# Kernel tuning notes

Hardware: AMD Instinct MI355X
Metric: run time of the kernel (lower is better)

The kernel has to match this reference:

```python
import jax, jax.numpy as jnp
import numpy as np

N_NODES = 100000
N_EDGES = 3200000
F_IN = 512
F_HID = 16
F_OUT = 40


def setup_inputs() -> dict:
    key = jax.random.key(0)
    k_x, k_e, k_w1, k_w2 = jax.random.split(key, 4)
    x = jax.random.normal(k_x, (N_NODES, F_IN), dtype=jnp.float32)
    edge_index = jax.random.randint(k_e, (2, N_EDGES), 0, N_NODES, dtype=jnp.int32)
    # Glorot-ish init for GCN weights
    W1 = jax.random.normal(k_w1, (F_IN, F_HID), dtype=jnp.float32) * (1.0 / np.sqrt(F_IN))
    b1 = jnp.zeros((F_HID,), dtype=jnp.float32)
    W2 = jax.random.normal(k_w2, (F_HID, F_OUT), dtype=jnp.float32) * (1.0 / np.sqrt(F_HID))
    b2 = jnp.zeros((F_OUT,), dtype=jnp.float32)
    return {"x": x, "edge_index": edge_index, "W1": W1, "b1": b1, "W2": W2, "b2": b2}


def reference(x, edge_index, W1, b1, W2, b2):
    # Eval-mode forward: dropout is identity.
    n = x.shape[0]
    loops = jnp.arange(n, dtype=edge_index.dtype)
    row = jnp.concatenate([edge_index[0], loops])  # sources (incl. self-loops)
    col = jnp.concatenate([edge_index[1], loops])  # targets
    # Symmetric GCN normalization: deg^{-1/2}[row] * deg^{-1/2}[col]
    deg = jax.ops.segment_sum(jnp.ones_like(row, dtype=x.dtype), col, num_segments=n)
    dinv = jnp.where(deg > 0, jax.lax.rsqrt(deg), 0.0).astype(x.dtype)
    norm = dinv[row] * dinv[col]  # [E+N]

    def gcn_conv(h, W, b):
        h = h @ W                                   # [N, F_out] dense transform first
        msg = h[row] * norm[:, None]                # gather + scale
        return jax.ops.segment_sum(msg, col, num_segments=n) + b  # scatter-add

    h = jax.nn.relu(gcn_conv(x, W1, b1))
    out = gcn_conv(h, W2, b2)
    return jax.nn.log_softmax(out, axis=1)
```

## Files before the change

### kernel.cpp

```cpp
#include <hip/hip_runtime.h>
#include <hip/hip_bf16.h>

#define F_IN  512
#define F_HID 16
#define F_OUT 40
#define CH    8192

typedef __attribute__((ext_vector_type(4))) float f32x4;
typedef __attribute__((ext_vector_type(8))) short s16x8;
typedef unsigned short ushort_t;

__device__ __forceinline__ float bf2f(ushort_t u) {
    union { unsigned u; float f; } v; v.u = (unsigned)u << 16; return v.f;
}
__device__ __forceinline__ ushort_t f2bf(float f) {
    __hip_bfloat16 h = __float2bfloat16(f);
    union { __hip_bfloat16 h; ushort_t u; } v; v.h = h; return v.u;
}


__global__ void k_zero_small(int* __restrict__ p, int n) {
    int i = threadIdx.x;
    if (i < n) p[i] = 0;
}

__global__ __launch_bounds__(256) void k_bhist(const int* __restrict__ col,
                                               int* __restrict__ bcnt, int nE) {
    __shared__ int bh[256];
    bh[threadIdx.x] = 0;
    __syncthreads();
    int base = blockIdx.x * CH;
    int end  = min(base + CH, nE);
    for (int e = base + threadIdx.x; e < end; e += 256)
        atomicAdd(&bh[col[e] >> 9], 1);
    __syncthreads();
    int v = bh[threadIdx.x];
    if (v) atomicAdd(&bcnt[threadIdx.x], v);
}

__global__ void k_bscan(const int* __restrict__ bcnt, int* __restrict__ bstart,
                        int* __restrict__ bcur, int nb, int nE) {
    __shared__ int s[256];
    int t = threadIdx.x;
    s[t] = (t < nb) ? bcnt[t] : 0;
    __syncthreads();
    for (int off = 1; off < 256; off <<= 1) {
        int v = (t >= off) ? s[t - off] : 0;
        __syncthreads();
        s[t] += v;
        __syncthreads();
    }
    int ex = (t == 0) ? 0 : s[t - 1];
    if (t < nb) { bstart[t] = ex; bcur[t] = ex; }
    if (t == nb) bstart[t] = nE;
}

__global__ __launch_bounds__(256) void k_bscatter(const int* __restrict__ row,
                                                  const int* __restrict__ colv,
                                                  int* __restrict__ bcur,
                                                  int* __restrict__ pairs, int nE) {
    __shared__ int colS[CH];
    __shared__ int bh[256];
    __shared__ int lcur[256];
    bh[threadIdx.x] = 0;
    __syncthreads();
    int base = blockIdx.x * CH;
    int end  = min(base + CH, nE);
    for (int e = base + threadIdx.x; e < end; e += 256) {
        int c = colv[e];
        colS[e - base] = c;
        atomicAdd(&bh[c >> 9], 1);
    }
    __syncthreads();
    int v = bh[threadIdx.x];
    if (v) lcur[threadIdx.x] = atomicAdd(&bcur[threadIdx.x], v);
    __syncthreads();
    for (int e = base + threadIdx.x; e < end; e += 256) {
        int c = colS[e - base];
        int pos = atomicAdd(&lcur[c >> 9], 1);
        pairs[pos] = (row[e] << 9) | (c & 511);
    }
}

__global__ __launch_bounds__(256) void k_build(const int* __restrict__ bstart,
                                               const int* __restrict__ pairs,
                                               int* __restrict__ start,
                                               int* __restrict__ csr,
                                               float* __restrict__ dinv,
                                               int n, int nE, int nbuck) {
    __shared__ int h[512];
    __shared__ int s[256];
    __shared__ int cur[512];
    int t = threadIdx.x;
    h[t] = 0; h[t + 256] = 0;
    __syncthreads();
    int s0 = bstart[blockIdx.x], s1 = bstart[blockIdx.x + 1];
    for (int e = s0 + t; e < s1; e += 256)
        atomicAdd(&h[pairs[e] & 511], 1);
    __syncthreads();
    int c0 = h[2 * t], c1 = h[2 * t + 1];
    int tsum = c0 + c1;
    s[t] = tsum;
    __syncthreads();
    for (int off = 1; off < 256; off <<= 1) {
        int v = (t >= off) ? s[t - off] : 0;
        __syncthreads();
        s[t] += v;
        __syncthreads();
    }
    int ex = s[t] - tsum;
    int st0 = s0 + ex, st1 = st0 + c0;
    int nbase = blockIdx.x << 9;
    int n0 = nbase + 2 * t, n1 = n0 + 1;
    if (n0 < n) { start[n0] = st0; dinv[n0] = rsqrtf((float)c0 + 1.0f); }
    if (n1 < n) { start[n1] = st1; dinv[n1] = rsqrtf((float)c1 + 1.0f); }
    cur[2 * t] = st0; cur[2 * t + 1] = st1;
    if (blockIdx.x == nbuck - 1 && t == 0) start[n] = nE;
    __syncthreads();
    for (int e = s0 + t; e < s1; e += 256) {
        int v = pairs[e];
        int pos = atomicAdd(&cur[v & 511], 1);
        csr[pos] = v >> 9;
    }
}

__global__ __launch_bounds__(256) void k_xw1(const float* __restrict__ x,
                                             const float* __restrict__ W1,
                                             const float* __restrict__ dinv,
                                             ushort_t* __restrict__ g1b, int n_tiles) {
    int lane = threadIdx.x & 63;
    int wid  = threadIdx.x >> 6;
    int m = lane & 15;
    int g = lane >> 4;

    s16x8 bf[16];
#pragma unroll
    for (int kb = 0; kb < 16; ++kb) {
        union { s16x8 s; unsigned u[4]; } bu;
#pragma unroll
        for (int p = 0; p < 4; ++p) {
            int k0 = kb * 32 + g * 8 + p * 2;
            float lo = W1[(k0 + 0) * F_HID + m];
            float hi = W1[(k0 + 1) * F_HID + m];
            unsigned pk;
            asm("v_cvt_pk_bf16_f32 %0, %1, %2" : "=v"(pk) : "v"(lo), "v"(hi));
            bu.u[p] = pk;
        }
        bf[kb] = bu.s;
    }

    int tile = blockIdx.x * 4 + wid;
    if (tile >= n_tiles) return;

    const float* xr = x + (size_t)(tile * 16 + m) * F_IN + g * 8;
    f32x4 acc = {0.f, 0.f, 0.f, 0.f};
#pragma unroll
    for (int kb = 0; kb < 16; ++kb) {
        f32x4 xa = *(const f32x4*)(xr + kb * 32);
        f32x4 xb = *(const f32x4*)(xr + kb * 32 + 4);
        union { s16x8 s; unsigned u[4]; } au;
        asm("v_cvt_pk_bf16_f32 %0, %1, %2" : "=v"(au.u[0]) : "v"(xa.x), "v"(xa.y));
        asm("v_cvt_pk_bf16_f32 %0, %1, %2" : "=v"(au.u[1]) : "v"(xa.z), "v"(xa.w));
        asm("v_cvt_pk_bf16_f32 %0, %1, %2" : "=v"(au.u[2]) : "v"(xb.x), "v"(xb.y));
        asm("v_cvt_pk_bf16_f32 %0, %1, %2" : "=v"(au.u[3]) : "v"(xb.z), "v"(xb.w));
        acc = __builtin_amdgcn_mfma_f32_16x16x32_bf16(au.s, bf[kb], acc, 0, 0, 0);
    }
#pragma unroll
    for (int p = 0; p < 4; ++p) {
        int rr = tile * 16 + g * 4 + p;
        g1b[(size_t)rr * F_HID + m] = f2bf(acc[p] * dinv[rr]);
    }
}

__global__ __launch_bounds__(256) void k_gather1(const int* __restrict__ start,
                                                 const int* __restrict__ csr,
                                                 const ushort_t* __restrict__ g1b,
                                                 const float* __restrict__ dinv,
                                                 const float* __restrict__ b1,
                                                 ushort_t* __restrict__ g2b, int n) {
    int wid = threadIdx.x >> 6, lane = threadIdx.x & 63;
    int node = blockIdx.x * 4 + wid;
    if (node >= n) return;
    int f = lane & 15, sub = lane >> 4;
    int s0 = start[node], s1 = start[node + 1];
    int len = s1 - s0;
    int q = (len + 3) >> 2;
    int beg = s0 + sub * q;
    int end = min(beg + q, s1);
    float a0 = 0.f, a1 = 0.f, a2 = 0.f, a3 = 0.f;
    int e = beg;
    for (; e + 4 <= end; e += 4) {
        int r0 = csr[e], r1 = csr[e + 1], r2 = csr[e + 2], r3 = csr[e + 3];
        a0 += bf2f(g1b[r0 * F_HID + f]);
        a1 += bf2f(g1b[r1 * F_HID + f]);
        a2 += bf2f(g1b[r2 * F_HID + f]);
        a3 += bf2f(g1b[r3 * F_HID + f]);
    }
    for (; e < end; ++e) a0 += bf2f(g1b[csr[e] * F_HID + f]);
    float acc = (a0 + a1) + (a2 + a3);
    acc += __shfl_xor(acc, 16);
    acc += __shfl_xor(acc, 32);
    acc += bf2f(g1b[(size_t)node * F_HID + f]);
    float di = dinv[node];
    float h = fmaxf(di * acc + b1[f], 0.f);
    if (sub == 0) g2b[(size_t)node * F_HID + f] = f2bf(di * h);
}

__global__ __launch_bounds__(256) void k_gather2f(const int* __restrict__ start,
                                                  const int* __restrict__ csr,
                                                  const ushort_t* __restrict__ g2b,
                                                  const float* __restrict__ dinv,
                                                  const float* __restrict__ W2,
                                                  const float* __restrict__ b2,
                                                  float* __restrict__ out, int n) {
    int wid = threadIdx.x >> 6, lane = threadIdx.x & 63;
    int node = blockIdx.x * 4 + wid;
    if (node >= n) return;
    int f = lane & 15, sub = lane >> 4;
    int j = (lane < F_OUT) ? lane : 0;

    float w2c[F_HID];
#pragma unroll
    for (int k = 0; k < F_HID; ++k) w2c[k] = W2[k * F_OUT + j];
    float bj = b2[j];

    int s0 = start[node], s1 = start[node + 1];
    int len = s1 - s0;
    int q = (len + 3) >> 2;
    int beg = s0 + sub * q;
    int end = min(beg + q, s1);
    float a0 = 0.f, a1 = 0.f, a2 = 0.f, a3 = 0.f;
    int e = beg;
    for (; e + 4 <= end; e += 4) {
        int r0 = csr[e], r1 = csr[e + 1], r2 = csr[e + 2], r3 = csr[e + 3];
        a0 += bf2f(g2b[r0 * F_HID + f]);
        a1 += bf2f(g2b[r1 * F_HID + f]);
        a2 += bf2f(g2b[r2 * F_HID + f]);
        a3 += bf2f(g2b[r3 * F_HID + f]);
    }
    for (; e < end; ++e) a0 += bf2f(g2b[csr[e] * F_HID + f]);
    float acc = (a0 + a1) + (a2 + a3);
    acc += __shfl_xor(acc, 16);
    acc += __shfl_xor(acc, 32);
    acc += bf2f(g2b[(size_t)node * F_HID + f]);
    float a = dinv[node] * acc;

    float o = bj;
#pragma unroll
    for (int k = 0; k < F_HID; ++k) o += __shfl(a, k) * w2c[k];

    float mo = (lane < F_OUT) ? o : -3.4e38f;
#pragma unroll
    for (int off = 32; off; off >>= 1) mo = fmaxf(mo, __shfl_xor(mo, off));
    float ev = (lane < F_OUT) ? __expf(o - mo) : 0.f;
    float sv = ev;
#pragma unroll
    for (int off = 32; off; off >>= 1) sv += __shfl_xor(sv, off);
    float lse = mo + __logf(sv);
    if (lane < F_OUT) out[(size_t)node * F_OUT + lane] = o - lse;
}


extern "C" void kernel_launch(void* const* d_in, const int* in_sizes, int n_in,
                              void* d_out, int out_size, void* d_ws, size_t ws_size,
                              hipStream_t stream) {
    const float* x  = (const float*)d_in[0];
    const int*   ei = (const int*)d_in[1];
    const float* W1 = (const float*)d_in[2];
    const float* b1 = (const float*)d_in[3];
    const float* W2 = (const float*)d_in[4];
    const float* b2 = (const float*)d_in[5];
    float* out = (float*)d_out;

    const int N = out_size / F_OUT;
    const int E = in_sizes[1] / 2;
    const int* row = ei;
    const int* col = ei + E;

    const int NBUCK = (N + 511) >> 9;
    const int NWGE  = (E + CH - 1) / CH;
    const int tiles = (N + 15) / 16;
    const int nbT   = (tiles + 3) / 4;
    const int nbG   = (N + 3) / 4;

    int* bcnt     = (int*)d_ws;
    int* bstart   = bcnt + 256;
    int* bcur     = bstart + 260;
    int* start    = bcur + 256;
    int* csr      = start + N + 4;
    int* pairs    = csr + E;
    float* dinv   = (float*)(pairs + E);
    ushort_t* g1b = (ushort_t*)(dinv + N);
    ushort_t* g2b = g1b + (size_t)N * F_HID;

    k_zero_small<<<1, 256, 0, stream>>>(bcnt, 256);
    k_bhist<<<NWGE, 256, 0, stream>>>(col, bcnt, E);
    k_bscan<<<1, 256, 0, stream>>>(bcnt, bstart, bcur, NBUCK, E);
    k_bscatter<<<NWGE, 256, 0, stream>>>(row, col, bcur, pairs, E);
    k_build<<<NBUCK, 256, 0, stream>>>(bstart, pairs, start, csr, dinv, N, E, NBUCK);

    k_xw1<<<nbT, 256, 0, stream>>>(x, W1, dinv, g1b, tiles);

    k_gather1<<<nbG, 256, 0, stream>>>(start, csr, g1b, dinv, b1, g2b, N);
    k_gather2f<<<nbG, 256, 0, stream>>>(start, csr, g2b, dinv, W2, b2, out, N);
}
```

Before: 260.1 us.

## Pack bf16 pairs in gathers, use 1024-thread CSR build and per-block histograms

The gather kernels now load two bf16 features per 32-bit word and split each node's edge list across 8 sub-groups instead of 4. This halves the number of load instructions per edge and adds memory-level parallelism. The CSR build kernels run with 1024-thread blocks, and the bucket histogram writes per-block counts that a scan kernel sums, which removes the zeroing kernel and the global atomics. In exchange, the gathers need an extra shuffle-reduction stage and the scan does a serial loop over blocks.

New measurement: 257.6 us. Within noise of the previous version (-1.0%).

```diff
diff --git a/kernel.cpp b/kernel.cpp
--- a/kernel.cpp
+++ b/kernel.cpp
@@ -9,40 +9,37 @@
 typedef __attribute__((ext_vector_type(4))) float f32x4;
 typedef __attribute__((ext_vector_type(8))) short s16x8;
 typedef unsigned short ushort_t;
-
-__device__ __forceinline__ float bf2f(ushort_t u) {
-    union { unsigned u; float f; } v; v.u = (unsigned)u << 16; return v.f;
-}
+typedef unsigned int uint_t;
+
+__device__ __forceinline__ float lof(uint_t v) { return __uint_as_float(v << 16); }
+__device__ __forceinline__ float hif(uint_t v) { return __uint_as_float(v & 0xffff0000u); }
 __device__ __forceinline__ ushort_t f2bf(float f) {
     __hip_bfloat16 h = __float2bfloat16(f);
     union { __hip_bfloat16 h; ushort_t u; } v; v.h = h; return v.u;
 }
 
 
-__global__ void k_zero_small(int* __restrict__ p, int n) {
-    int i = threadIdx.x;
-    if (i < n) p[i] = 0;
-}
-
-__global__ __launch_bounds__(256) void k_bhist(const int* __restrict__ col,
-                                               int* __restrict__ bcnt, int nE) {
+__global__ __launch_bounds__(1024) void k_bhist(const int* __restrict__ col,
+                                                int* __restrict__ bhall, int nE) {
     __shared__ int bh[256];
-    bh[threadIdx.x] = 0;
+    int t = threadIdx.x;
+    if (t < 256) bh[t] = 0;
     __syncthreads();
     int base = blockIdx.x * CH;
     int end  = min(base + CH, nE);
-    for (int e = base + threadIdx.x; e < end; e += 256)
+    for (int e = base + t; e < end; e += 1024)
         atomicAdd(&bh[col[e] >> 9], 1);
     __syncthreads();
-    int v = bh[threadIdx.x];
-    if (v) atomicAdd(&bcnt[threadIdx.x], v);
-}
-
-__global__ void k_bscan(const int* __restrict__ bcnt, int* __restrict__ bstart,
-                        int* __restrict__ bcur, int nb, int nE) {
+    if (t < 256) bhall[blockIdx.x * 256 + t] = bh[t];
+}
+
+__global__ void k_bscan2(const int* __restrict__ bhall, int* __restrict__ bstart,
+                         int* __restrict__ bcur, int nwge) {
     __shared__ int s[256];
     int t = threadIdx.x;
-    s[t] = (t < nb) ? bcnt[t] : 0;
+    int sum = 0;
+    for (int w = 0; w < nwge; ++w) sum += bhall[w * 256 + t];
+    s[t] = sum;
     __syncthreads();
     for (int off = 1; off < 256; off <<= 1) {
         int v = (t >= off) ? s[t - off] : 0;
@@ -50,74 +47,80 @@
         s[t] += v;
         __syncthreads();
     }
-    int ex = (t == 0) ? 0 : s[t - 1];
-    if (t < nb) { bstart[t] = ex; bcur[t] = ex; }
-    if (t == nb) bstart[t] = nE;
-}
-
-__global__ __launch_bounds__(256) void k_bscatter(const int* __restrict__ row,
-                                                  const int* __restrict__ colv,
-                                                  int* __restrict__ bcur,
-                                                  int* __restrict__ pairs, int nE) {
+    int ex = s[t] - sum;
+    bstart[t] = ex;
+    bcur[t] = ex;
+    if (t == 255) bstart[256] = s[255];
+}
+
+__global__ __launch_bounds__(1024) void k_bscatter(const int* __restrict__ row,
+                                                   const int* __restrict__ colv,
+                                                   int* __restrict__ bcur,
+                                                   int* __restrict__ pairs, int nE) {
     __shared__ int colS[CH];
     __shared__ int bh[256];
     __shared__ int lcur[256];
-    bh[threadIdx.x] = 0;
+    int t = threadIdx.x;
+    if (t < 256) bh[t] = 0;
     __syncthreads();
     int base = blockIdx.x * CH;
     int end  = min(base + CH, nE);
-    for (int e = base + threadIdx.x; e < end; e += 256) {
+    for (int e = base + t; e < end; e += 1024) {
         int c = colv[e];
         colS[e - base] = c;
         atomicAdd(&bh[c >> 9], 1);
     }
     __syncthreads();
-    int v = bh[threadIdx.x];
-    if (v) lcur[threadIdx.x] = atomicAdd(&bcur[threadIdx.x], v);
-    __syncthreads();
-    for (int e = base + threadIdx.x; e < end; e += 256) {
+    if (t < 256) {
+        int v = bh[t];
+        if (v) lcur[t] = atomicAdd(&bcur[t], v);
+    }
+    __syncthreads();
+    for (int e = base + t; e < end; e += 1024) {
         int c = colS[e - base];
         int pos = atomicAdd(&lcur[c >> 9], 1);
         pairs[pos] = (row[e] << 9) | (c & 511);
     }
 }
 
-__global__ __launch_bounds__(256) void k_build(const int* __restrict__ bstart,
-                                               const int* __restrict__ pairs,
-                                               int* __restrict__ start,
-                                               int* __restrict__ csr,
-                                               float* __restrict__ dinv,
-                                               int n, int nE, int nbuck) {
+__global__ __launch_bounds__(1024) void k_build(const int* __restrict__ bstart,
+                                                const int* __restrict__ pairs,
+                                                int* __restrict__ start,
+                                                int* __restrict__ csr,
+                                                float* __restrict__ dinv,
+                                                int n, int nE) {
     __shared__ int h[512];
-    __shared__ int s[256];
+    __shared__ int s[512];
     __shared__ int cur[512];
     int t = threadIdx.x;
-    h[t] = 0; h[t + 256] = 0;
+    if (t < 512) h[t] = 0;
     __syncthreads();
     int s0 = bstart[blockIdx.x], s1 = bstart[blockIdx.x + 1];
-    for (int e = s0 + t; e < s1; e += 256)
+    for (int e = s0 + t; e < s1; e += 1024)
         atomicAdd(&h[pairs[e] & 511], 1);
     __syncthreads();
-    int c0 = h[2 * t], c1 = h[2 * t + 1];
-    int tsum = c0 + c1;
-    s[t] = tsum;
-    __syncthreads();
-    for (int off = 1; off < 256; off <<= 1) {
-        int v = (t >= off) ? s[t - off] : 0;
+    if (t < 512) s[t] = h[t];
+    __syncthreads();
+    for (int off = 1; off < 512; off <<= 1) {
+        int v = 0;
+        if (t < 512 && t >= off) v = s[t - off];
         __syncthreads();
-        s[t] += v;
+        if (t < 512) s[t] += v;
         __syncthreads();
     }
-    int ex = s[t] - tsum;
-    int st0 = s0 + ex, st1 = st0 + c0;
-    int nbase = blockIdx.x << 9;
-    int n0 = nbase + 2 * t, n1 = n0 + 1;
-    if (n0 < n) { start[n0] = st0; dinv[n0] = rsqrtf((float)c0 + 1.0f); }
-    if (n1 < n) { start[n1] = st1; dinv[n1] = rsqrtf((float)c1 + 1.0f); }
-    cur[2 * t] = st0; cur[2 * t + 1] = st1;
-    if (blockIdx.x == nbuck - 1 && t == 0) start[n] = nE;
-    __syncthreads();
-    for (int e = s0 + t; e < s1; e += 256) {
+    if (t < 512) {
+        int c = h[t];
+        int st = s0 + s[t] - c;
+        int node = (blockIdx.x << 9) + t;
+        if (node < n) {
+            start[node] = st;
+            dinv[node] = rsqrtf((float)c + 1.0f);
+        }
+        cur[t] = st;
+    }
+    if (blockIdx.x == 0 && t == 0) start[n] = nE;
+    __syncthreads();
+    for (int e = s0 + t; e < s1; e += 1024) {
         int v = pairs[e];
         int pos = atomicAdd(&cur[v & 511], 1);
         csr[pos] = v >> 9;
@@ -174,41 +177,55 @@
 
 __global__ __launch_bounds__(256) void k_gather1(const int* __restrict__ start,
                                                  const int* __restrict__ csr,
-                                                 const ushort_t* __restrict__ g1b,
+                                                 const uint_t* __restrict__ g1,
                                                  const float* __restrict__ dinv,
                                                  const float* __restrict__ b1,
-                                                 ushort_t* __restrict__ g2b, int n) {
+                                                 uint_t* __restrict__ g2, int n) {
     int wid = threadIdx.x >> 6, lane = threadIdx.x & 63;
     int node = blockIdx.x * 4 + wid;
     if (node >= n) return;
-    int f = lane & 15, sub = lane >> 4;
+    int fp = lane & 7, sub = lane >> 3;
     int s0 = start[node], s1 = start[node + 1];
     int len = s1 - s0;
-    int q = (len + 3) >> 2;
-    int beg = s0 + sub * q;
-    int end = min(beg + q, s1);
-    float a0 = 0.f, a1 = 0.f, a2 = 0.f, a3 = 0.f;
-    int e = beg;
+    int q = (len + 7) >> 3;
+    int e = s0 + sub * q;
+    int end = min(e + q, s1);
+    float l0 = 0.f, h0 = 0.f, l1 = 0.f, h1 = 0.f, l2 = 0.f, h2 = 0.f, l3 = 0.f, h3 = 0.f;
     for (; e + 4 <= end; e += 4) {
         int r0 = csr[e], r1 = csr[e + 1], r2 = csr[e + 2], r3 = csr[e + 3];
-        a0 += bf2f(g1b[r0 * F_HID + f]);
-        a1 += bf2f(g1b[r1 * F_HID + f]);
-        a2 += bf2f(g1b[r2 * F_HID + f]);
-        a3 += bf2f(g1b[r3 * F_HID + f]);
-    }
-    for (; e < end; ++e) a0 += bf2f(g1b[csr[e] * F_HID + f]);
-    float acc = (a0 + a1) + (a2 + a3);
-    acc += __shfl_xor(acc, 16);
-    acc += __shfl_xor(acc, 32);
-    acc += bf2f(g1b[(size_t)node * F_HID + f]);
+        uint_t v0 = g1[r0 * 8 + fp], v1 = g1[r1 * 8 + fp];
+        uint_t v2 = g1[r2 * 8 + fp], v3 = g1[r3 * 8 + fp];
+        l0 += lof(v0); h0 += hif(v0);
+        l1 += lof(v1); h1 += hif(v1);
+        l2 += lof(v2); h2 += hif(v2);
+        l3 += lof(v3); h3 += hif(v3);
+    }
+    for (; e < end; ++e) {
+        uint_t v = g1[csr[e] * 8 + fp];
+        l0 += lof(v); h0 += hif(v);
+    }
+    float alo = (l0 + l1) + (l2 + l3);
+    float ahi = (h0 + h1) + (h2 + h3);
+    alo += __shfl_xor(alo, 8);  ahi += __shfl_xor(ahi, 8);
+    alo += __shfl_xor(alo, 16); ahi += __shfl_xor(ahi, 16);
+    alo += __shfl_xor(alo, 32); ahi += __shfl_xor(ahi, 32);
+    uint_t sv = g1[(size_t)node * 8 + fp];
+    alo += lof(sv); ahi += hif(sv);
     float di = dinv[node];
-    float h = fmaxf(di * acc + b1[f], 0.f);
-    if (sub == 0) g2b[(size_t)node * F_HID + f] = f2bf(di * h);
+    const float2* b1v = (const float2*)b1;
+    float2 bb = b1v[fp];
+    float hlo = fmaxf(di * alo + bb.x, 0.f) * di;
+    float hhi = fmaxf(di * ahi + bb.y, 0.f) * di;
+    if (sub == 0) {
+        unsigned pk;
+        asm("v_cvt_pk_bf16_f32 %0, %1, %2" : "=v"(pk) : "v"(hlo), "v"(hhi));
+        g2[(size_t)node * 8 + fp] = pk;
+    }
 }
 
 __global__ __launch_bounds__(256) void k_gather2f(const int* __restrict__ start,
                                                   const int* __restrict__ csr,
-                                                  const ushort_t* __restrict__ g2b,
+                                                  const uint_t* __restrict__ g2,
                                                   const float* __restrict__ dinv,
                                                   const float* __restrict__ W2,
                                                   const float* __restrict__ b2,
@@ -216,7 +233,7 @@
     int wid = threadIdx.x >> 6, lane = threadIdx.x & 63;
     int node = blockIdx.x * 4 + wid;
     if (node >= n) return;
-    int f = lane & 15, sub = lane >> 4;
+    int fp = lane & 7, sub = lane >> 3;
     int j = (lane < F_OUT) ? lane : 0;
 
     float w2c[F_HID];
@@ -226,37 +243,48 @@
 
     int s0 = start[node], s1 = start[node + 1];
     int len = s1 - s0;
-    int q = (len + 3) >> 2;
-    int beg = s0 + sub * q;
-    int end = min(beg + q, s1);
-    float a0 = 0.f, a1 = 0.f, a2 = 0.f, a3 = 0.f;
-    int e = beg;
+    int q = (len + 7) >> 3;
+    int e = s0 + sub * q;
+    int end = min(e + q, s1);
+    float l0 = 0.f, h0 = 0.f, l1 = 0.f, h1 = 0.f, l2 = 0.f, h2 = 0.f, l3 = 0.f, h3 = 0.f;
     for (; e + 4 <= end; e += 4) {
         int r0 = csr[e], r1 = csr[e + 1], r2 = csr[e + 2], r3 = csr[e + 3];
-        a0 += bf2f(g2b[r0 * F_HID + f]);
-        a1 += bf2f(g2b[r1 * F_HID + f]);
-        a2 += bf2f(g2b[r2 * F_HID + f]);
-        a3 += bf2f(g2b[r3 * F_HID + f]);
-    }
-    for (; e < end; ++e) a0 += bf2f(g2b[csr[e] * F_HID + f]);
-    float acc = (a0 + a1) + (a2 + a3);
-    acc += __shfl_xor(acc, 16);
-    acc += __shfl_xor(acc, 32);
-    acc += bf2f(g2b[(size_t)node * F_HID + f]);
-    float a = dinv[node] * acc;
+        uint_t v0 = g2[r0 * 8 + fp], v1 = g2[r1 * 8 + fp];
+        uint_t v2 = g2[r2 * 8 + fp], v3 = g2[r3 * 8 + fp];
+        l0 += lof(v0); h0 += hif(v0);
+        l1 += lof(v1); h1 += hif(v1);
+        l2 += lof(v2); h2 += hif(v2);
+        l3 += lof(v3); h3 += hif(v3);
+    }
+    for (; e < end; ++e) {
+        uint_t v = g2[csr[e] * 8 + fp];
+        l0 += lof(v); h0 += hif(v);
+    }
+    float alo = (l0 + l1) + (l2 + l3);
+    float ahi = (h0 + h1) + (h2 + h3);
+    alo += __shfl_xor(alo, 8);  ahi += __shfl_xor(ahi, 8);
+    alo += __shfl_xor(alo, 16); ahi += __shfl_xor(ahi, 16);
+    alo += __shfl_xor(alo, 32); ahi += __shfl_xor(ahi, 32);
+    uint_t sv = g2[(size_t)node * 8 + fp];
+    alo += lof(sv); ahi += hif(sv);
+    float di = dinv[node];
+    float a_lo = di * alo;
+    float a_hi = di * ahi;
 
     float o = bj;
 #pragma unroll
-    for (int k = 0; k < F_HID; ++k) o += __shfl(a, k) * w2c[k];
+    for (int k = 0; k < F_HID; k += 2) {
+        o += __shfl(a_lo, k >> 1) * w2c[k] + __shfl(a_hi, k >> 1) * w2c[k + 1];
+    }
 
     float mo = (lane < F_OUT) ? o : -3.4e38f;
 #pragma unroll
     for (int off = 32; off; off >>= 1) mo = fmaxf(mo, __shfl_xor(mo, off));
     float ev = (lane < F_OUT) ? __expf(o - mo) : 0.f;
-    float sv = ev;
-#pragma unroll
-    for (int off = 32; off; off >>= 1) sv += __shfl_xor(sv, off);
-    float lse = mo + __logf(sv);
+    float sv2 = ev;
+#pragma unroll
+    for (int off = 32; off; off >>= 1) sv2 += __shfl_xor(sv2, off);
+    float lse = mo + __logf(sv2);
     if (lane < F_OUT) out[(size_t)node * F_OUT + lane] = o - lse;
 }
 
@@ -283,24 +311,23 @@
     const int nbT   = (tiles + 3) / 4;
     const int nbG   = (N + 3) / 4;
 
-    int* bcnt     = (int*)d_ws;
-    int* bstart   = bcnt + 256;
+    int* bstart   = (int*)d_ws;
     int* bcur     = bstart + 260;
-    int* start    = bcur + 256;
+    int* bhall    = bcur + 256;
+    int* start    = bhall + NWGE * 256;
     int* csr      = start + N + 4;
     int* pairs    = csr + E;
     float* dinv   = (float*)(pairs + E);
-    ushort_t* g1b = (ushort_t*)(dinv + N);
-    ushort_t* g2b = g1b + (size_t)N * F_HID;
-
-    k_zero_small<<<1, 256, 0, stream>>>(bcnt, 256);
-    k_bhist<<<NWGE, 256, 0, stream>>>(col, bcnt, E);
-    k_bscan<<<1, 256, 0, stream>>>(bcnt, bstart, bcur, NBUCK, E);
-    k_bscatter<<<NWGE, 256, 0, stream>>>(row, col, bcur, pairs, E);
-    k_build<<<NBUCK, 256, 0, stream>>>(bstart, pairs, start, csr, dinv, N, E, NBUCK);
-
-    k_xw1<<<nbT, 256, 0, stream>>>(x, W1, dinv, g1b, tiles);
-
-    k_gather1<<<nbG, 256, 0, stream>>>(start, csr, g1b, dinv, b1, g2b, N);
-    k_gather2f<<<nbG, 256, 0, stream>>>(start, csr, g2b, dinv, W2, b2, out, N);
-}
+    uint_t* g1    = (uint_t*)(dinv + N);
+    uint_t* g2    = g1 + (size_t)N * 8;
+
+    k_bhist<<<NWGE, 1024, 0, stream>>>(col, bhall, E);
+    k_bscan2<<<1, 256, 0, stream>>>(bhall, bstart, bcur, NWGE);
+    k_bscatter<<<NWGE, 1024, 0, stream>>>(row, col, bcur, pairs, E);
+    k_build<<<NBUCK, 1024, 0, stream>>>(bstart, pairs, start, csr, dinv, N, E);
+
+    k_xw1<<<nbT, 256, 0, stream>>>(x, W1, dinv, (ushort_t*)g1, tiles);
+
+    k_gather1<<<nbG, 256, 0, stream>>>(start, csr, g1, dinv, b1, g2, N);
+    k_gather2f<<<nbG, 256, 0, stream>>>(start, csr, g2, dinv, W2, b2, out, N);
+}
```
